# Kernel tuning notes

Measured on AMD Instinct MI355X. Metric: run time of the kernel, lower is better.

## Reference

```python
import jax, jax.numpy as jnp
import numpy as np

N = 100000   # nodes
E = 1600000  # edges (avg degree 16)
D = 64       # out_channels (in_channels == out_channels, so no zero-padding step)
L = 2        # GatedGraphConv num_layers


def setup_inputs() -> dict:
    key = jax.random.key(0)
    ks = jax.random.split(key, 11)
    w = lambda k, shape: jax.random.normal(k, shape, jnp.float32) * 0.05
    return {
        "x": jax.random.normal(ks[0], (N, D), jnp.float32),
        "edge_index": jax.random.randint(ks[1], (2, E), 0, N, dtype=jnp.int64),
        "conv_w": w(ks[2], (L, D, D)),        # GatedGraphConv per-layer message weight
        "gru_w_ih": w(ks[3], (3 * D, D)),     # GRUCell input->hidden (r|z|n)
        "gru_w_hh": w(ks[4], (3 * D, D)),     # GRUCell hidden->hidden (r|z|n)
        "gru_b_ih": w(ks[5], (3 * D,)),
        "gru_b_hh": w(ks[6], (3 * D,)),
        "lin_w": w(ks[7], (D, D)),            # nn.Linear(out, out)
        "lin_b": w(ks[8], (D,)),
        "attn_w": w(ks[9], (1, D)),           # nn.Linear(out, 1)
        "attn_b": w(ks[10], (1,)),
    }


def reference(x, edge_index, conv_w, gru_w_ih, gru_w_hh, gru_b_ih, gru_b_hh,
              lin_w, lin_b, attn_w, attn_b):
    src, dst = edge_index[0], edge_index[1]
    h = x  # in_channels == out_channels -> no padding
    for i in range(L):
        m = h @ conv_w[i]  # [N, D] transformed messages
        # gather at source nodes, scatter-add into target nodes
        agg = jax.ops.segment_sum(m[src], dst, num_segments=N)  # [N, D]
        # GRUCell(agg, h)
        gi = agg @ gru_w_ih.T + gru_b_ih  # [N, 3D]
        gh = h @ gru_w_hh.T + gru_b_hh    # [N, 3D]
        i_r, i_z, i_n = jnp.split(gi, 3, axis=1)
        h_r, h_z, h_n = jnp.split(gh, 3, axis=1)
        r = jax.nn.sigmoid(i_r + h_r)
        z = jax.nn.sigmoid(i_z + h_z)
        n = jnp.tanh(i_n + r * h_n)
        h = (1.0 - z) * n + z * h
    y = jax.nn.relu(h) @ lin_w.T + lin_b                 # [N, D]
    attn = jax.nn.softmax(y @ attn_w.T + attn_b, axis=0) # [N, 1], softmax over nodes
    return (attn * y).sum(axis=0, keepdims=True)          # [1, D]
```

## Files before the change

### kernel.cpp

```cpp
#include <hip/hip_runtime.h>


typedef __attribute__((ext_vector_type(8))) short s8v;
typedef __attribute__((ext_vector_type(4))) float f32x4;

#define CSR_CAP 12288
#define HSTR 136

__device__ __forceinline__ unsigned short f32_bf16_rn(float x) {
  unsigned u = __float_as_uint(x);
  u += 0x7FFF + ((u >> 16) & 1);
  return (unsigned short)(u >> 16);
}

__device__ __forceinline__ int wave_incl_scan(int v, int lane) {
#pragma unroll
  for (int d = 1; d < 64; d <<= 1) {
    int u = __shfl_up(v, d);
    if (lane >= d) v += u;
  }
  return v;
}

__device__ __forceinline__ int detect_is64(const int* ei, int E) {
  int nz = 0;
  int lim = (E < 512) ? E : 512;
  for (int i = threadIdx.x; i < lim; i += blockDim.x)
    nz |= (ei[2 * i + 1] != 0);
  return __syncthreads_or(nz) ? 0 : 1;
}

__device__ __forceinline__ void load_edge(const int* ei, int E, int is64,
                                          int e, int& s, int& d) {
  if (is64) { s = ei[2 * e]; d = ei[2 * (E + e)]; }
  else      { s = ei[e];     d = ei[E + e]; }
}

__global__ __launch_bounds__(256) void count_kernel(
    const int* __restrict__ ei, int E,
    int* __restrict__ G, int P, int perBlk, int NB) {
  __shared__ int hist[512];
  int tid = threadIdx.x, b = blockIdx.x;
  for (int i = tid; i < 512; i += 256) hist[i] = 0;
  int is64 = detect_is64(ei, E);
  __syncthreads();
  int e0 = b * perBlk, e1 = min(e0 + perBlk, E);
  for (int e = e0 + tid; e < e1; e += 256) {
    int s, d; load_edge(ei, E, is64, e, s, d);
    atomicAdd(&hist[d >> 8], 1);
  }
  __syncthreads();
  for (int i = tid; i < P; i += 256) G[i * NB + b] = hist[i];
}

__global__ __launch_bounds__(256) void scan2a(int* __restrict__ G,
                                              int* __restrict__ total, int NB) {
  __shared__ int wsum[4];
  int p = blockIdx.x, tid = threadIdx.x, lane = tid & 63, wv = tid >> 6;
  int v = G[p * NB + tid];
  int incl = wave_incl_scan(v, lane);
  if (lane == 63) wsum[wv] = incl;
  __syncthreads();
  if (tid == 0) {
    int a = wsum[0], b2 = wsum[1], c = wsum[2], d = wsum[3];
    total[p] = a + b2 + c + d;
    wsum[0] = 0; wsum[1] = a; wsum[2] = a + b2; wsum[3] = a + b2 + c;
  }
  __syncthreads();
  G[p * NB + tid] = incl - v + wsum[wv];
}

__global__ void scan2b(const int* __restrict__ total, int* __restrict__ partStart,
                       int P) {
  int lane = threadIdx.x;
  int running = 0;
  for (int base = 0; base < P; base += 64) {
    int idx = base + lane;
    int v = (idx < P) ? total[idx] : 0;
    int incl = wave_incl_scan(v, lane);
    int tot = __shfl(incl, 63);
    if (idx < P) partStart[idx] = running + incl - v;
    running += tot;
  }
  if (lane == 0) partStart[P] = running;
}

__global__ __launch_bounds__(256) void scatter_kernel(
    const int* __restrict__ ei, int E,
    const int* __restrict__ G, const int* __restrict__ partStart,
    int* __restrict__ bucket, int P, int perBlk, int NB) {
  __shared__ int cur[512];
  int tid = threadIdx.x, b = blockIdx.x;
  int is64 = detect_is64(ei, E);
  for (int i = tid; i < P; i += 256) cur[i] = partStart[i] + G[i * NB + b];
  __syncthreads();
  int e0 = b * perBlk, e1 = min(e0 + perBlk, E);
  for (int e = e0 + tid; e < e1; e += 256) {
    int s, d; load_edge(ei, E, is64, e, s, d);
    int pos = atomicAdd(&cur[d >> 8], 1);
    bucket[pos] = ((d & 255) << 17) | s;
  }
}

__global__ __launch_bounds__(256) void buildcsr_kernel(
    const int* __restrict__ partStart, const int* __restrict__ bucket,
    int* __restrict__ row_ptr, int* __restrict__ col, int N) {
  __shared__ int stage[CSR_CAP];
  __shared__ int hist[256];
  __shared__ int cur[256];
  __shared__ int wsum[4];
  int p = blockIdx.x, tid = threadIdx.x;
  int beg = partStart[p], end = partStart[p + 1];
  int cnt = end - beg;
  int base = p << 8;
  hist[tid] = 0;
  __syncthreads();
  bool staged = (cnt <= CSR_CAP);
  if (staged) {
    for (int i = tid; i < cnt; i += 256) {
      int v = bucket[beg + i];
      stage[i] = v;
      atomicAdd(&hist[(v >> 17) & 255], 1);
    }
  } else {
    for (int i = tid; i < cnt; i += 256)
      atomicAdd(&hist[(bucket[beg + i] >> 17) & 255], 1);
  }
  __syncthreads();
  int lane = tid & 63, wv = tid >> 6;
  int v = hist[tid];
  int incl = wave_incl_scan(v, lane);
  if (lane == 63) wsum[wv] = incl;
  __syncthreads();
  if (tid == 0) {
    int s0 = wsum[0], s1 = wsum[1], s2 = wsum[2];
    wsum[0] = 0; wsum[1] = s0; wsum[2] = s0 + s1; wsum[3] = s0 + s1 + s2;
  }
  __syncthreads();
  int excl = incl - v + wsum[wv];
  cur[tid] = beg + excl;
  if (base + tid < N) {
    if (tid == 0) row_ptr[base] = beg;
    row_ptr[base + tid + 1] = beg + excl + v;
  }
  __syncthreads();
  if (staged) {
    for (int i = tid; i < cnt; i += 256) {
      int v2 = stage[i];
      int pos = atomicAdd(&cur[(v2 >> 17) & 255], 1);
      col[pos] = v2 & 0x1FFFF;
    }
  } else {
    for (int i = tid; i < cnt; i += 256) {
      int v2 = bucket[beg + i];
      int pos = atomicAdd(&cur[(v2 >> 17) & 255], 1);
      col[pos] = v2 & 0x1FFFF;
    }
  }
}

__global__ void wprep_kernel(const float* __restrict__ conv_w,
                             const float* __restrict__ w_ih,
                             const float* __restrict__ whh,
                             const float* __restrict__ lin_w,
                             unsigned short* __restrict__ Bt,
                             unsigned short* __restrict__ Lt) {
  int idx = blockIdx.x * blockDim.x + threadIdx.x;
  if (idx < 65536) {
    int l = idx >> 15;
    int rr = idx & 32767;
    int cp = rr >> 7, p = rr & 127;
    int ch = cp >> 2, g = cp & 3;
    float val = 0.f;
    if (p < 64) {
      int j = (g == 0) ? ch : (g == 1) ? 64 + ch : (g == 2) ? 128 + ch : -1;
      if (j >= 0) {
        const float* C = conv_w + l * 4096 + p * 64;
        const float* W = w_ih + j * 64;
#pragma unroll 8
        for (int k = 0; k < 64; k++) val += C[k] * W[k];
      }
    } else {
      int q = p - 64;
      if (g == 0)      val = whh[ch * 64 + q];
      else if (g == 1) val = whh[(64 + ch) * 64 + q];
      else if (g == 3) val = whh[(128 + ch) * 64 + q];
    }
    Bt[(size_t)l * 32768 + (size_t)cp * 128 + p] = f32_bf16_rn(val);
  } else if (idx < 65536 + 4096) {
    int i2 = idx - 65536;
    float val = lin_w[i2];
    unsigned short hi = f32_bf16_rn(val);
    float fh = __uint_as_float((unsigned)hi << 16);
    unsigned short lo = f32_bf16_rn(val - fh);
    Lt[i2] = hi;
    Lt[4096 + i2] = lo;
  }
}

__global__ __launch_bounds__(256) void cvt16_kernel(
    const float* __restrict__ in, unsigned short* __restrict__ out, int n8) {
  int idx = blockIdx.x * blockDim.x + threadIdx.x;
  if (idx >= n8) return;
  const float4* p = (const float4*)(in + (size_t)idx * 8);
  float4 v0 = p[0], v1 = p[1];
  uint4 o;
  o.x = (unsigned)f32_bf16_rn(v0.x) | ((unsigned)f32_bf16_rn(v0.y) << 16);
  o.y = (unsigned)f32_bf16_rn(v0.z) | ((unsigned)f32_bf16_rn(v0.w) << 16);
  o.z = (unsigned)f32_bf16_rn(v1.x) | ((unsigned)f32_bf16_rn(v1.y) << 16);
  o.w = (unsigned)f32_bf16_rn(v1.z) | ((unsigned)f32_bf16_rn(v1.w) << 16);
  *(uint4*)(out + (size_t)idx * 8) = o;
}

__device__ __forceinline__ void acc_u2(unsigned rx, unsigned ry, float4& a) {
  a.x += __uint_as_float(rx << 16);
  a.y += __uint_as_float(rx & 0xFFFF0000u);
  a.z += __uint_as_float(ry << 16);
  a.w += __uint_as_float(ry & 0xFFFF0000u);
}

__global__ __launch_bounds__(256) void gather_kernel(
    const unsigned short* __restrict__ hb, const int* __restrict__ row_ptr,
    const int* __restrict__ col, unsigned short* __restrict__ sout,
    int N, int Em1) {
  int gt = blockIdx.x * blockDim.x + threadIdx.x;
  int n = gt >> 6, lane = gt & 63;
  if (n >= N) return;
  int grp = lane >> 4, q = lane & 15;
  int beg = row_ptr[n], end = row_ptr[n + 1];
  float4 acc = make_float4(0.f, 0.f, 0.f, 0.f);

  {
    int safe0 = min(beg, Em1);
    uint2 r[8];
    int idx[8];
#pragma unroll
    for (int i = 0; i < 8; i++) {
      int ee = beg + grp + 4 * i;
      idx[i] = (ee < end) ? ee : -1;
      int ci = (idx[i] >= 0) ? ee : safe0;
      int s = col[ci];
      r[i] = *(const uint2*)(hb + (size_t)s * 64 + q * 4);
    }
#pragma unroll
    for (int i = 0; i < 8; i++)
      if (idx[i] >= 0) acc_u2(r[i].x, r[i].y, acc);
  }
  for (int ee = beg + grp + 32; ee < end; ee += 4) {
    int s = col[ee];
    uint2 r = *(const uint2*)(hb + (size_t)s * 64 + q * 4);
    acc_u2(r.x, r.y, acc);
  }

#pragma unroll
  for (int off = 16; off <= 32; off <<= 1) {
    acc.x += __shfl_xor(acc.x, off);
    acc.y += __shfl_xor(acc.y, off);
    acc.z += __shfl_xor(acc.z, off);
    acc.w += __shfl_xor(acc.w, off);
  }
  if (grp == 0) {
    uint2 o;
    o.x = (unsigned)f32_bf16_rn(acc.x) | ((unsigned)f32_bf16_rn(acc.y) << 16);
    o.y = (unsigned)f32_bf16_rn(acc.z) | ((unsigned)f32_bf16_rn(acc.w) << 16);
    *(uint2*)(sout + (size_t)n * 64 + q * 4) = o;
  }
}

__global__ __launch_bounds__(512, 4) void gemm_gru_kernel(
    const unsigned short* __restrict__ s16,
    const unsigned short* __restrict__ h16in,
    unsigned short* __restrict__ h16out,
    const unsigned short* __restrict__ bt,
    const float* __restrict__ b_ih, const float* __restrict__ b_hh,
    int N, int ntiles) {
  __shared__ short Ahi[64 * HSTR];
  const int tid = threadIdx.x;
  const int lane = tid & 63, w = tid >> 6;
  const int l15 = lane & 15, ko = (lane >> 4) * 8;
  const int q = lane >> 4;

  s8v Bf[2][4];
#pragma unroll
  for (int ct = 0; ct < 2; ct++)
#pragma unroll
    for (int kk = 0; kk < 4; kk++)
      Bf[ct][kk] = *(const s8v*)(bt + (size_t)(32 * w + 16 * ct + l15) * 128 +
                                 kk * 32 + ko);

  const int ch0 = 8 * w + q, ch1 = ch0 + 4;
  const float br0 = b_ih[ch0] + b_hh[ch0], br1 = b_ih[ch1] + b_hh[ch1];
  const float bz0 = b_ih[64 + ch0] + b_hh[64 + ch0], bz1 = b_ih[64 + ch1] + b_hh[64 + ch1];
  const float bi0 = b_ih[128 + ch0], bi1 = b_ih[128 + ch1];
  const float bn0 = b_hh[128 + ch0], bn1 = b_hh[128 + ch1];

  const int g = tid >> 3, qc = tid & 7;

  for (int tile = blockIdx.x; tile < ntiles; tile += gridDim.x) {
    const int nb = tile * 64;
    const int node = nb + g;
    {
      uint4 sv = make_uint4(0, 0, 0, 0), hv = make_uint4(0, 0, 0, 0);
      if (node < N) {
        sv = *(const uint4*)(s16 + (size_t)node * 64 + qc * 8);
        hv = *(const uint4*)(h16in + (size_t)node * 64 + qc * 8);
      }
      *(uint4*)&Ahi[g * HSTR + qc * 8] = sv;
      *(uint4*)&Ahi[g * HSTR + 64 + qc * 8] = hv;
    }
    __syncthreads();

    f32x4 acc[4][2];
#pragma unroll
    for (int m = 0; m < 4; m++)
#pragma unroll
      for (int ct = 0; ct < 2; ct++) acc[m][ct] = (f32x4)(0.f);

#pragma unroll
    for (int m = 0; m < 4; m++) {
      const short* arh = &Ahi[(16 * m + l15) * HSTR + ko];
#pragma unroll
      for (int kk = 0; kk < 4; kk++) {
        s8v a_h = *(const s8v*)(arh + kk * 32);
#pragma unroll
        for (int ct = 0; ct < 2; ct++)
          acc[m][ct] = __builtin_amdgcn_mfma_f32_16x16x32_bf16(Bf[ct][kk], a_h, acc[m][ct], 0, 0, 0);
      }
    }

#pragma unroll
    for (int m = 0; m < 4; m++) {
      int loc = 16 * m + l15;
      int nd = nb + loc;
      if (nd < N) {
#pragma unroll
        for (int ct = 0; ct < 2; ct++) {
          int ch = ct ? ch1 : ch0;
          unsigned hu = (unsigned short)Ahi[loc * HSTR + 64 + ch];
          float hold = __uint_as_float(hu << 16);
          float rr = 1.f / (1.f + __expf(-(acc[m][ct][0] + (ct ? br1 : br0))));
          float zz = 1.f / (1.f + __expf(-(acc[m][ct][1] + (ct ? bz1 : bz0))));
          float narg = acc[m][ct][2] + (ct ? bi1 : bi0) +
                       rr * (acc[m][ct][3] + (ct ? bn1 : bn0));
          narg = fminf(fmaxf(narg, -15.f), 15.f);
          float t = __expf(2.f * narg);
          float nn = (t - 1.f) / (t + 1.f);
          float hv = (1.f - zz) * nn + zz * hold;
          h16out[(size_t)nd * 64 + ch] = f32_bf16_rn(hv);
        }
      }
    }
    __syncthreads();
  }
}

__device__ __forceinline__ unsigned relu_pk_bf16(unsigned v) {
  unsigned lo = (v & 0x00008000u) ? 0u : (v & 0x0000FFFFu);
  unsigned hi = (v & 0x80000000u) ? 0u : (v & 0xFFFF0000u);
  return lo | hi;
}

__global__ __launch_bounds__(256, 2) void final_mfma(
    const unsigned short* __restrict__ h16, const unsigned short* __restrict__ Lt,
    const float* __restrict__ lin_b, const float* __restrict__ attn_w,
    const float* __restrict__ attn_b, float* __restrict__ partials,
    int N, int ntiles) {
  __shared__ short Alds[64 * 72];
  __shared__ float red[4][64];
  __shared__ float pl[64];
  const int tid = threadIdx.x;
  const int lane = tid & 63, w = tid >> 6;
  const int l15 = lane & 15, ko = (lane >> 4) * 8;
  const int q = lane >> 4;

  s8v Lh[2], Ll[2];
  const int col = 16 * w + l15;
#pragma unroll
  for (int kk = 0; kk < 2; kk++) {
    Lh[kk] = *(const s8v*)(Lt + (size_t)col * 64 + kk * 32 + ko);
    Ll[kk] = *(const s8v*)(Lt + 4096 + (size_t)col * 64 + kk * 32 + ko);
  }
  const float lb = lin_b[col];
  const float aw = attn_w[col];
  const float ab = attn_b[0];
  const int sr = tid >> 2, part = tid & 3;

  float accS = 0.f;
  float accY = 0.f;

  for (int tile = blockIdx.x; tile < ntiles; tile += gridDim.x) {
    const int nb = tile * 64;
    {
      int node = nb + sr;
      uint4 v0 = make_uint4(0, 0, 0, 0), v1 = make_uint4(0, 0, 0, 0);
      if (node < N) {
        v0 = *(const uint4*)(h16 + (size_t)node * 64 + part * 16);
        v1 = *(const uint4*)(h16 + (size_t)node * 64 + part * 16 + 8);
      }
      v0.x = relu_pk_bf16(v0.x); v0.y = relu_pk_bf16(v0.y);
      v0.z = relu_pk_bf16(v0.z); v0.w = relu_pk_bf16(v0.w);
      v1.x = relu_pk_bf16(v1.x); v1.y = relu_pk_bf16(v1.y);
      v1.z = relu_pk_bf16(v1.z); v1.w = relu_pk_bf16(v1.w);
      short* ah = &Alds[sr * 72 + part * 16];
      *(uint4*)ah = v0;
      *(uint4*)(ah + 8) = v1;
    }
    __syncthreads();

    f32x4 acc[4];
#pragma unroll
    for (int m = 0; m < 4; m++) acc[m] = (f32x4)(0.f);
#pragma unroll
    for (int m = 0; m < 4; m++) {
      const short* arow = &Alds[(16 * m + l15) * 72 + ko];
#pragma unroll
      for (int kk = 0; kk < 2; kk++) {
        s8v a_h = *(const s8v*)(arow + kk * 32);
        acc[m] = __builtin_amdgcn_mfma_f32_16x16x32_bf16(a_h, Lh[kk], acc[m], 0, 0, 0);
        acc[m] = __builtin_amdgcn_mfma_f32_16x16x32_bf16(a_h, Ll[kk], acc[m], 0, 0, 0);
      }
    }
    __syncthreads();

    float cc[4][4];
#pragma unroll
    for (int m = 0; m < 4; m++)
#pragma unroll
      for (int g = 0; g < 4; g++) cc[m][g] = (acc[m][g] + lb) * aw;
#pragma unroll
    for (int off = 1; off <= 8; off <<= 1)
#pragma unroll
      for (int m = 0; m < 4; m++)
#pragma unroll
        for (int g = 0; g < 4; g++) cc[m][g] += __shfl_xor(cc[m][g], off);
    if (l15 == 0) {
#pragma unroll
      for (int m = 0; m < 4; m++)
#pragma unroll
        for (int g = 0; g < 4; g++) red[w][16 * m + 4 * q + g] = cc[m][g];
    }
    __syncthreads();
    if (tid < 64) {
      float t = red[0][tid] + red[1][tid] + red[2][tid] + red[3][tid] + ab;
      float p = (nb + tid < N) ? __expf(t) : 0.f;
      pl[tid] = p;
      accS += p;
    }
    __syncthreads();
#pragma unroll
    for (int m = 0; m < 4; m++)
#pragma unroll
      for (int g = 0; g < 4; g++)
        accY += pl[16 * m + 4 * q + g] * (acc[m][g] + lb);
  }

  accY += __shfl_xor(accY, 16);
  accY += __shfl_xor(accY, 32);
  if (lane < 16) partials[(size_t)blockIdx.x * 66 + 16 * w + lane] = accY;
  if (w == 0) {
    float s = accS;
#pragma unroll
    for (int off = 1; off < 64; off <<= 1) s += __shfl_xor(s, off);
    if (lane == 0) partials[(size_t)blockIdx.x * 66 + 64] = s;
  }
}

__global__ void final_p2(const float* __restrict__ partials,
                         float* __restrict__ out, int nb) {
  __shared__ float red[16][65];
  int tid = threadIdx.x;
  int j = tid & 63, grp = tid >> 6;
  float sy = 0.f, ss = 0.f;
  for (int b = grp; b < nb; b += 16) {
    sy += partials[b * 66 + j];
    if (j == 0) ss += partials[b * 66 + 64];
  }
  red[grp][j] = sy;
  if (j == 0) red[grp][64] = ss;
  __syncthreads();
  if (tid < 64) {
    float Y = 0.f, S = 0.f;
#pragma unroll
    for (int i = 0; i < 16; i++) { Y += red[i][tid]; S += red[i][64]; }
    out[tid] = Y / S;
  }
}

extern "C" void kernel_launch(void* const* d_in, const int* in_sizes, int n_in,
                              void* d_out, int out_size, void* d_ws, size_t ws_size,
                              hipStream_t stream) {
  const float* x       = (const float*)d_in[0];
  const int*   ei      = (const int*)d_in[1];
  const float* conv_w  = (const float*)d_in[2];
  const float* gw_ih   = (const float*)d_in[3];
  const float* gw_hh   = (const float*)d_in[4];
  const float* gb_ih   = (const float*)d_in[5];
  const float* gb_hh   = (const float*)d_in[6];
  const float* lin_w   = (const float*)d_in[7];
  const float* lin_b   = (const float*)d_in[8];
  const float* attn_w  = (const float*)d_in[9];
  const float* attn_b  = (const float*)d_in[10];
  float* out = (float*)d_out;

  const int N = in_sizes[0] / 64;
  const int E = in_sizes[1] / 2;
  const int P  = (N + 255) >> 8;
  const int NB = 256;
  const int perBlk = (E + NB - 1) / NB;

  char* ws = (char*)d_ws;
  size_t off = 0;
  auto alloc = [&](size_t bytes) {
    void* p = ws + off;
    off = (off + bytes + 255) & ~(size_t)255;
    return p;
  };
  int*   G         = (int*)alloc((size_t)P * NB * 4);
  int*   total     = (int*)alloc((size_t)P * 4);
  int*   partStart = (int*)alloc((size_t)(P + 1) * 4);
  int*   bucket    = (int*)alloc((size_t)E * 4);
  int*   row_ptr   = (int*)alloc((size_t)(N + 1) * 4);
  int*   colb      = (int*)alloc((size_t)E * 4);
  unsigned short* Bt  = (unsigned short*)alloc(2 * 256 * 128 * 2);
  unsigned short* Lt  = (unsigned short*)alloc(2 * 4096 * 2);
  unsigned short* b16x = (unsigned short*)alloc((size_t)N * 64 * 2);
  unsigned short* b16h = (unsigned short*)alloc((size_t)N * 64 * 2);
  unsigned short* s16  = (unsigned short*)alloc((size_t)N * 64 * 2);
  float* partials  = (float*)alloc(1024 * 66 * 4);
  if (off > ws_size) return;

  count_kernel<<<NB, 256, 0, stream>>>(ei, E, G, P, perBlk, NB);
  scan2a<<<P, 256, 0, stream>>>(G, total, NB);
  scan2b<<<1, 64, 0, stream>>>(total, partStart, P);
  scatter_kernel<<<NB, 256, 0, stream>>>(ei, E, G, partStart, bucket, P, perBlk, NB);
  buildcsr_kernel<<<P, 256, 0, stream>>>(partStart, bucket, row_ptr, colb, N);
  wprep_kernel<<<(65536 + 4096 + 255) / 256, 256, 0, stream>>>(conv_w, gw_ih, gw_hh,
                                                               lin_w, Bt, Lt);
  int n8 = (N * 64) / 8;
  cvt16_kernel<<<(n8 + 255) / 256, 256, 0, stream>>>(x, b16x, n8);

  int gb = (N * 64 + 255) / 256;
  int ntiles = (N + 63) / 64;
  gather_kernel<<<gb, 256, 0, stream>>>(b16x, row_ptr, colb, s16, N, E - 1);
  gemm_gru_kernel<<<1024, 512, 0, stream>>>(s16, b16x, b16h, Bt,
                                            gb_ih, gb_hh, N, ntiles);
  gather_kernel<<<gb, 256, 0, stream>>>(b16h, row_ptr, colb, s16, N, E - 1);
  gemm_gru_kernel<<<1024, 512, 0, stream>>>(s16, b16h, b16h, Bt + 32768,
                                            gb_ih, gb_hh, N, ntiles);
  final_mfma<<<512, 256, 0, stream>>>(b16h, Lt, lin_b, attn_w, attn_b, partials, N, ntiles);
  final_p2<<<1, 1024, 0, stream>>>(partials, out, 512);
}
```

Baseline: 217.3 us.

## Double-buffer GRU GEMM tile loads via global_load_lds and fuse tail kernels

New measurement: 250.8 us. +15.4%, slower.

```diff
diff --git a/kernel.cpp b/kernel.cpp
--- a/kernel.cpp
+++ b/kernel.cpp
@@ -5,7 +5,6 @@
 typedef __attribute__((ext_vector_type(4))) float f32x4;
 
 #define CSR_CAP 12288
-#define HSTR 136
 
 __device__ __forceinline__ unsigned short f32_bf16_rn(float x) {
   unsigned u = __float_as_uint(x);
@@ -38,9 +37,10 @@
 
 __global__ __launch_bounds__(256) void count_kernel(
     const int* __restrict__ ei, int E,
-    int* __restrict__ G, int P, int perBlk, int NB) {
+    int* __restrict__ G, int P, int perBlk, int NB, int* __restrict__ dcnt) {
   __shared__ int hist[512];
   int tid = threadIdx.x, b = blockIdx.x;
+  if (b == 0 && tid < 2) dcnt[tid] = 0;
   for (int i = tid; i < 512; i += 256) hist[i] = 0;
   int is64 = detect_is64(ei, E);
   __syncthreads();
@@ -54,8 +54,12 @@
 }
 
 __global__ __launch_bounds__(256) void scan2a(int* __restrict__ G,
-                                              int* __restrict__ total, int NB) {
+                                              int* __restrict__ total,
+                                              int* __restrict__ partStart,
+                                              int NB, int P,
+                                              int* __restrict__ dcnt) {
   __shared__ int wsum[4];
+  __shared__ int amLast;
   int p = blockIdx.x, tid = threadIdx.x, lane = tid & 63, wv = tid >> 6;
   int v = G[p * NB + tid];
   int incl = wave_incl_scan(v, lane);
@@ -68,21 +72,23 @@
   }
   __syncthreads();
   G[p * NB + tid] = incl - v + wsum[wv];
-}
-
-__global__ void scan2b(const int* __restrict__ total, int* __restrict__ partStart,
-                       int P) {
-  int lane = threadIdx.x;
-  int running = 0;
-  for (int base = 0; base < P; base += 64) {
-    int idx = base + lane;
-    int v = (idx < P) ? total[idx] : 0;
-    int incl = wave_incl_scan(v, lane);
-    int tot = __shfl(incl, 63);
-    if (idx < P) partStart[idx] = running + incl - v;
-    running += tot;
-  }
-  if (lane == 0) partStart[P] = running;
+  if (tid == 0) {
+    __threadfence();
+    amLast = (atomicAdd(&dcnt[0], 1) == P - 1);
+  }
+  __syncthreads();
+  if (amLast && tid < 64) {
+    int running = 0;
+    for (int base = 0; base < P; base += 64) {
+      int idx = base + lane;
+      int vv = (idx < P) ? total[idx] : 0;
+      int ii = wave_incl_scan(vv, lane);
+      int tot = __shfl(ii, 63);
+      if (idx < P) partStart[idx] = running + ii - vv;
+      running += tot;
+    }
+    if (lane == 0) partStart[P] = running;
+  }
 }
 
 __global__ __launch_bounds__(256) void scatter_kernel(
@@ -163,8 +169,10 @@
                              const float* __restrict__ w_ih,
                              const float* __restrict__ whh,
                              const float* __restrict__ lin_w,
+                             const float* __restrict__ x,
                              unsigned short* __restrict__ Bt,
-                             unsigned short* __restrict__ Lt) {
+                             unsigned short* __restrict__ Lt,
+                             unsigned short* __restrict__ x16, int n8) {
   int idx = blockIdx.x * blockDim.x + threadIdx.x;
   if (idx < 65536) {
     int l = idx >> 15;
@@ -195,21 +203,19 @@
     unsigned short lo = f32_bf16_rn(val - fh);
     Lt[i2] = hi;
     Lt[4096 + i2] = lo;
-  }
-}
-
-__global__ __launch_bounds__(256) void cvt16_kernel(
-    const float* __restrict__ in, unsigned short* __restrict__ out, int n8) {
-  int idx = blockIdx.x * blockDim.x + threadIdx.x;
-  if (idx >= n8) return;
-  const float4* p = (const float4*)(in + (size_t)idx * 8);
-  float4 v0 = p[0], v1 = p[1];
-  uint4 o;
-  o.x = (unsigned)f32_bf16_rn(v0.x) | ((unsigned)f32_bf16_rn(v0.y) << 16);
-  o.y = (unsigned)f32_bf16_rn(v0.z) | ((unsigned)f32_bf16_rn(v0.w) << 16);
-  o.z = (unsigned)f32_bf16_rn(v1.x) | ((unsigned)f32_bf16_rn(v1.y) << 16);
-  o.w = (unsigned)f32_bf16_rn(v1.z) | ((unsigned)f32_bf16_rn(v1.w) << 16);
-  *(uint4*)(out + (size_t)idx * 8) = o;
+  } else {
+    int i2 = idx - (65536 + 4096);
+    if (i2 < n8) {
+      const float4* pp = (const float4*)(x + (size_t)i2 * 8);
+      float4 v0 = pp[0], v1 = pp[1];
+      uint4 o;
+      o.x = (unsigned)f32_bf16_rn(v0.x) | ((unsigned)f32_bf16_rn(v0.y) << 16);
+      o.y = (unsigned)f32_bf16_rn(v0.z) | ((unsigned)f32_bf16_rn(v0.w) << 16);
+      o.z = (unsigned)f32_bf16_rn(v1.x) | ((unsigned)f32_bf16_rn(v1.y) << 16);
+      o.w = (unsigned)f32_bf16_rn(v1.z) | ((unsigned)f32_bf16_rn(v1.w) << 16);
+      *(uint4*)(x16 + (size_t)i2 * 8) = o;
+    }
+  }
 }
 
 __device__ __forceinline__ void acc_u2(unsigned rx, unsigned ry, float4& a) {
@@ -274,7 +280,7 @@
     const unsigned short* __restrict__ bt,
     const float* __restrict__ b_ih, const float* __restrict__ b_hh,
     int N, int ntiles) {
-  __shared__ short Ahi[64 * HSTR];
+  __shared__ short Alds[2 * 8192];
   const int tid = threadIdx.x;
   const int lane = tid & 63, w = tid >> 6;
   const int l15 = lane & 15, ko = (lane >> 4) * 8;
@@ -294,21 +300,36 @@
   const float bi0 = b_ih[128 + ch0], bi1 = b_ih[128 + ch1];
   const float bn0 = b_hh[128 + ch0], bn1 = b_hh[128 + ch1];
 
-  const int g = tid >> 3, qc = tid & 7;
-
-  for (int tile = blockIdx.x; tile < ntiles; tile += gridDim.x) {
-    const int nb = tile * 64;
-    const int node = nb + g;
-    {
-      uint4 sv = make_uint4(0, 0, 0, 0), hv = make_uint4(0, 0, 0, 0);
-      if (node < N) {
-        sv = *(const uint4*)(s16 + (size_t)node * 64 + qc * 8);
-        hv = *(const uint4*)(h16in + (size_t)node * 64 + qc * 8);
-      }
-      *(uint4*)&Ahi[g * HSTR + qc * 8] = sv;
-      *(uint4*)&Ahi[g * HSTR + 64 + qc * 8] = hv;
-    }
+  const int lrow = lane >> 3;
+  const int schk = (lane & 7) ^ lrow;
+  const int stride = gridDim.x;
+
+  auto issue_loads = [&](int tile, int buf) {
+    int node = min(tile * 64 + 8 * w + lrow, N - 1);
+    const unsigned short* gs = s16 + (size_t)node * 64 + schk * 8;
+    const unsigned short* gh = h16in + (size_t)node * 64 + schk * 8;
+    short* ds = &Alds[buf * 8192 + w * 512];
+    short* dh = &Alds[buf * 8192 + 4096 + w * 512];
+    __builtin_amdgcn_global_load_lds(
+        (const __attribute__((address_space(1))) void*)gs,
+        (__attribute__((address_space(3))) void*)ds, 16, 0, 0);
+    __builtin_amdgcn_global_load_lds(
+        (const __attribute__((address_space(1))) void*)gh,
+        (__attribute__((address_space(3))) void*)dh, 16, 0, 0);
+  };
+
+  const int tile0 = blockIdx.x;
+  if (tile0 < ntiles) issue_loads(tile0, 0);
+  int cur = 0;
+
+  for (int tile = tile0; tile < ntiles; tile += stride) {
     __syncthreads();
+    const int nxt = tile + stride;
+    if (nxt < ntiles) issue_loads(nxt, cur ^ 1);
+
+    const short* sp = &Alds[cur * 8192];
+    const short* hp = sp + 4096;
+    const int rx = l15 & 7;
 
     f32x4 acc[4][2];
 #pragma unroll
@@ -318,16 +339,19 @@
 
 #pragma unroll
     for (int m = 0; m < 4; m++) {
-      const short* arh = &Ahi[(16 * m + l15) * HSTR + ko];
+      const int r = 16 * m + l15;
 #pragma unroll
       for (int kk = 0; kk < 4; kk++) {
-        s8v a_h = *(const s8v*)(arh + kk * 32);
+        const short* base = (kk < 2) ? sp : hp;
+        int cc = (((kk & 1) * 4 + q) ^ rx);
+        s8v a_h = *(const s8v*)(base + r * 64 + cc * 8);
 #pragma unroll
         for (int ct = 0; ct < 2; ct++)
           acc[m][ct] = __builtin_amdgcn_mfma_f32_16x16x32_bf16(Bf[ct][kk], a_h, acc[m][ct], 0, 0, 0);
       }
     }
 
+    const int nb = tile * 64;
 #pragma unroll
     for (int m = 0; m < 4; m++) {
       int loc = 16 * m + l15;
@@ -336,7 +360,8 @@
 #pragma unroll
         for (int ct = 0; ct < 2; ct++) {
           int ch = ct ? ch1 : ch0;
-          unsigned hu = (unsigned short)Ahi[loc * HSTR + 64 + ch];
+          int hcc = (ch >> 3) ^ rx;
+          unsigned hu = (unsigned short)hp[loc * 64 + hcc * 8 + (ch & 7)];
           float hold = __uint_as_float(hu << 16);
           float rr = 1.f / (1.f + __expf(-(acc[m][ct][0] + (ct ? br1 : br0))));
           float zz = 1.f / (1.f + __expf(-(acc[m][ct][1] + (ct ? bz1 : bz0))));
@@ -350,7 +375,7 @@
         }
       }
     }
-    __syncthreads();
+    cur ^= 1;
   }
 }
 
@@ -364,10 +389,11 @@
     const unsigned short* __restrict__ h16, const unsigned short* __restrict__ Lt,
     const float* __restrict__ lin_b, const float* __restrict__ attn_w,
     const float* __restrict__ attn_b, float* __restrict__ partials,
-    int N, int ntiles) {
+    float* __restrict__ out, int* __restrict__ dcnt, int N, int ntiles) {
   __shared__ short Alds[64 * 72];
   __shared__ float red[4][64];
   __shared__ float pl[64];
+  __shared__ int amLast;
   const int tid = threadIdx.x;
   const int lane = tid & 63, w = tid >> 6;
   const int l15 = lane & 15, ko = (lane >> 4) * 8;
@@ -463,26 +489,28 @@
     for (int off = 1; off < 64; off <<= 1) s += __shfl_xor(s, off);
     if (lane == 0) partials[(size_t)blockIdx.x * 66 + 64] = s;
   }
-}
-
-__global__ void final_p2(const float* __restrict__ partials,
-                         float* __restrict__ out, int nb) {
-  __shared__ float red[16][65];
-  int tid = threadIdx.x;
-  int j = tid & 63, grp = tid >> 6;
-  float sy = 0.f, ss = 0.f;
-  for (int b = grp; b < nb; b += 16) {
-    sy += partials[b * 66 + j];
-    if (j == 0) ss += partials[b * 66 + 64];
-  }
-  red[grp][j] = sy;
-  if (j == 0) red[grp][64] = ss;
-  __syncthreads();
-  if (tid < 64) {
-    float Y = 0.f, S = 0.f;
-#pragma unroll
-    for (int i = 0; i < 16; i++) { Y += red[i][tid]; S += red[i][64]; }
-    out[tid] = Y / S;
+
+  if (tid == 0) {
+    __threadfence();
+    amLast = (atomicAdd(&dcnt[1], 1) == (int)gridDim.x - 1);
+  }
+  __syncthreads();
+  if (amLast) {
+    __shared__ float red2[4][65];
+    int grp = tid >> 6, j = tid & 63;
+    float sy = 0.f, ss = 0.f;
+    for (int b = grp; b < (int)gridDim.x; b += 4) {
+      sy += partials[(size_t)b * 66 + j];
+      if (j == 0) ss += partials[(size_t)b * 66 + 64];
+    }
+    red2[grp][j] = sy;
+    if (j == 0) red2[grp][64] = ss;
+    __syncthreads();
+    if (tid < 64) {
+      float Y = red2[0][tid] + red2[1][tid] + red2[2][tid] + red2[3][tid];
+      float S = red2[0][64] + red2[1][64] + red2[2][64] + red2[3][64];
+      out[tid] = Y / S;
+    }
   }
 }
 
@@ -521,6 +549,7 @@
   int*   bucket    = (int*)alloc((size_t)E * 4);
   int*   row_ptr   = (int*)alloc((size_t)(N + 1) * 4);
   int*   colb      = (int*)alloc((size_t)E * 4);
+  int*   dcnt      = (int*)alloc(256);
   unsigned short* Bt  = (unsigned short*)alloc(2 * 256 * 128 * 2);
   unsigned short* Lt  = (unsigned short*)alloc(2 * 4096 * 2);
   unsigned short* b16x = (unsigned short*)alloc((size_t)N * 64 * 2);
@@ -529,15 +558,13 @@
   float* partials  = (float*)alloc(1024 * 66 * 4);
   if (off > ws_size) return;
 
-  count_kernel<<<NB, 256, 0, stream>>>(ei, E, G, P, perBlk, NB);
-  scan2a<<<P, 256, 0, stream>>>(G, total, NB);
-  scan2b<<<1, 64, 0, stream>>>(total, partStart, P);
+  count_kernel<<<NB, 256, 0, stream>>>(ei, E, G, P, perBlk, NB, dcnt);
+  scan2a<<<P, 256, 0, stream>>>(G, total, partStart, NB, P, dcnt);
   scatter_kernel<<<NB, 256, 0, stream>>>(ei, E, G, partStart, bucket, P, perBlk, NB);
   buildcsr_kernel<<<P, 256, 0, stream>>>(partStart, bucket, row_ptr, colb, N);
-  wprep_kernel<<<(65536 + 4096 + 255) / 256, 256, 0, stream>>>(conv_w, gw_ih, gw_hh,
-                                                               lin_w, Bt, Lt);
   int n8 = (N * 64) / 8;
-  cvt16_kernel<<<(n8 + 255) / 256, 256, 0, stream>>>(x, b16x, n8);
+  wprep_kernel<<<(65536 + 4096 + n8 + 255) / 256, 256, 0, stream>>>(
+      conv_w, gw_ih, gw_hh, lin_w, x, Bt, Lt, b16x, n8);
 
   int gb = (N * 64 + 255) / 256;
   int ntiles = (N + 63) / 64;
@@ -547,6 +574,6 @@
   gather_kernel<<<gb, 256, 0, stream>>>(b16h, row_ptr, colb, s16, N, E - 1);
   gemm_gru_kernel<<<1024, 512, 0, stream>>>(s16, b16h, b16h, Bt + 32768,
                                             gb_ih, gb_hh, N, ntiles);
-  final_mfma<<<512, 256, 0, stream>>>(b16h, Lt, lin_b, attn_w, attn_b, partials, N, ntiles);
-  final_p2<<<1, 1024, 0, stream>>>(partials, out, 512);
-}
+  final_mfma<<<512, 256, 0, stream>>>(b16h, Lt, lin_b, attn_w, attn_b,
+                                      partials, out, dcnt, N, ntiles);
+}
```

## Fold final linear layer through attention sum and fuse small prep kernels

Applied to the files above, without the earlier changes.

New measurement: 229.3 us. 5.5% more time.

```diff
diff --git a/kernel.cpp b/kernel.cpp
--- a/kernel.cpp
+++ b/kernel.cpp
@@ -38,9 +38,10 @@
 
 __global__ __launch_bounds__(256) void count_kernel(
     const int* __restrict__ ei, int E,
-    int* __restrict__ G, int P, int perBlk, int NB) {
+    int* __restrict__ G, int P, int perBlk, int NB, int* __restrict__ dcnt) {
   __shared__ int hist[512];
   int tid = threadIdx.x, b = blockIdx.x;
+  if (b == 0 && tid == 0) dcnt[0] = 0;
   for (int i = tid; i < 512; i += 256) hist[i] = 0;
   int is64 = detect_is64(ei, E);
   __syncthreads();
@@ -54,8 +55,12 @@
 }
 
 __global__ __launch_bounds__(256) void scan2a(int* __restrict__ G,
-                                              int* __restrict__ total, int NB) {
+                                              int* __restrict__ total,
+                                              int* __restrict__ partStart,
+                                              int NB, int P,
+                                              int* __restrict__ dcnt) {
   __shared__ int wsum[4];
+  __shared__ int amLast;
   int p = blockIdx.x, tid = threadIdx.x, lane = tid & 63, wv = tid >> 6;
   int v = G[p * NB + tid];
   int incl = wave_incl_scan(v, lane);
@@ -68,21 +73,23 @@
   }
   __syncthreads();
   G[p * NB + tid] = incl - v + wsum[wv];
-}
-
-__global__ void scan2b(const int* __restrict__ total, int* __restrict__ partStart,
-                       int P) {
-  int lane = threadIdx.x;
-  int running = 0;
-  for (int base = 0; base < P; base += 64) {
-    int idx = base + lane;
-    int v = (idx < P) ? total[idx] : 0;
-    int incl = wave_incl_scan(v, lane);
-    int tot = __shfl(incl, 63);
-    if (idx < P) partStart[idx] = running + incl - v;
-    running += tot;
-  }
-  if (lane == 0) partStart[P] = running;
+  if (tid == 0) {
+    __threadfence();
+    amLast = (atomicAdd(&dcnt[0], 1) == P - 1);
+  }
+  __syncthreads();
+  if (amLast && tid < 64) {
+    int running = 0;
+    for (int base = 0; base < P; base += 64) {
+      int idx = base + lane;
+      int vv = (idx < P) ? total[idx] : 0;
+      int ii = wave_incl_scan(vv, lane);
+      int tot = __shfl(ii, 63);
+      if (idx < P) partStart[idx] = running + ii - vv;
+      running += tot;
+    }
+    if (lane == 0) partStart[P] = running;
+  }
 }
 
 __global__ __launch_bounds__(256) void scatter_kernel(
@@ -163,8 +170,11 @@
                              const float* __restrict__ w_ih,
                              const float* __restrict__ whh,
                              const float* __restrict__ lin_w,
+                             const float* __restrict__ attn_w,
+                             const float* __restrict__ x,
                              unsigned short* __restrict__ Bt,
-                             unsigned short* __restrict__ Lt) {
+                             float* __restrict__ uf,
+                             unsigned short* __restrict__ x16, int n8) {
   int idx = blockIdx.x * blockDim.x + threadIdx.x;
   if (idx < 65536) {
     int l = idx >> 15;
@@ -187,29 +197,25 @@
       else if (g == 3) val = whh[(128 + ch) * 64 + q];
     }
     Bt[(size_t)l * 32768 + (size_t)cp * 128 + p] = f32_bf16_rn(val);
-  } else if (idx < 65536 + 4096) {
-    int i2 = idx - 65536;
-    float val = lin_w[i2];
-    unsigned short hi = f32_bf16_rn(val);
-    float fh = __uint_as_float((unsigned)hi << 16);
-    unsigned short lo = f32_bf16_rn(val - fh);
-    Lt[i2] = hi;
-    Lt[4096 + i2] = lo;
-  }
-}
-
-__global__ __launch_bounds__(256) void cvt16_kernel(
-    const float* __restrict__ in, unsigned short* __restrict__ out, int n8) {
-  int idx = blockIdx.x * blockDim.x + threadIdx.x;
-  if (idx >= n8) return;
-  const float4* p = (const float4*)(in + (size_t)idx * 8);
-  float4 v0 = p[0], v1 = p[1];
-  uint4 o;
-  o.x = (unsigned)f32_bf16_rn(v0.x) | ((unsigned)f32_bf16_rn(v0.y) << 16);
-  o.y = (unsigned)f32_bf16_rn(v0.z) | ((unsigned)f32_bf16_rn(v0.w) << 16);
-  o.z = (unsigned)f32_bf16_rn(v1.x) | ((unsigned)f32_bf16_rn(v1.y) << 16);
-  o.w = (unsigned)f32_bf16_rn(v1.z) | ((unsigned)f32_bf16_rn(v1.w) << 16);
-  *(uint4*)(out + (size_t)idx * 8) = o;
+  } else if (idx < 65536 + 64) {
+    int k = idx - 65536;
+    float acc = 0.f;
+#pragma unroll 8
+    for (int c = 0; c < 64; c++) acc += attn_w[c] * lin_w[c * 64 + k];
+    uf[k] = acc;
+  } else if (idx >= 65792) {
+    int i2 = idx - 65792;
+    if (i2 < n8) {
+      const float4* pp = (const float4*)(x + (size_t)i2 * 8);
+      float4 v0 = pp[0], v1 = pp[1];
+      uint4 o;
+      o.x = (unsigned)f32_bf16_rn(v0.x) | ((unsigned)f32_bf16_rn(v0.y) << 16);
+      o.y = (unsigned)f32_bf16_rn(v0.z) | ((unsigned)f32_bf16_rn(v0.w) << 16);
+      o.z = (unsigned)f32_bf16_rn(v1.x) | ((unsigned)f32_bf16_rn(v1.y) << 16);
+      o.w = (unsigned)f32_bf16_rn(v1.z) | ((unsigned)f32_bf16_rn(v1.w) << 16);
+      *(uint4*)(x16 + (size_t)i2 * 8) = o;
+    }
+  }
 }
 
 __device__ __forceinline__ void acc_u2(unsigned rx, unsigned ry, float4& a) {
@@ -360,129 +366,96 @@
   return lo | hi;
 }
 
-__global__ __launch_bounds__(256, 2) void final_mfma(
-    const unsigned short* __restrict__ h16, const unsigned short* __restrict__ Lt,
-    const float* __restrict__ lin_b, const float* __restrict__ attn_w,
-    const float* __restrict__ attn_b, float* __restrict__ partials,
-    int N, int ntiles) {
-  __shared__ short Alds[64 * 72];
-  __shared__ float red[4][64];
-  __shared__ float pl[64];
-  const int tid = threadIdx.x;
-  const int lane = tid & 63, w = tid >> 6;
-  const int l15 = lane & 15, ko = (lane >> 4) * 8;
-  const int q = lane >> 4;
-
-  s8v Lh[2], Ll[2];
-  const int col = 16 * w + l15;
-#pragma unroll
-  for (int kk = 0; kk < 2; kk++) {
-    Lh[kk] = *(const s8v*)(Lt + (size_t)col * 64 + kk * 32 + ko);
-    Ll[kk] = *(const s8v*)(Lt + 4096 + (size_t)col * 64 + kk * 32 + ko);
-  }
-  const float lb = lin_b[col];
-  const float aw = attn_w[col];
-  const float ab = attn_b[0];
-  const int sr = tid >> 2, part = tid & 3;
-
+__global__ __launch_bounds__(256) void attn_stream(
+    const unsigned short* __restrict__ h16, const float* __restrict__ u,
+    float* __restrict__ partials, int N) {
+  __shared__ float zb[4][64];
+  __shared__ float sb[4];
+  int tid = threadIdx.x, lane = tid & 63, wv = tid >> 6;
+  int g = lane >> 3, c8 = lane & 7;
+  float u8[8];
+#pragma unroll
+  for (int i = 0; i < 8; i++) u8[i] = u[c8 * 8 + i];
+  float accY[8];
+#pragma unroll
+  for (int i = 0; i < 8; i++) accY[i] = 0.f;
   float accS = 0.f;
-  float accY = 0.f;
-
-  for (int tile = blockIdx.x; tile < ntiles; tile += gridDim.x) {
-    const int nb = tile * 64;
-    {
-      int node = nb + sr;
-      uint4 v0 = make_uint4(0, 0, 0, 0), v1 = make_uint4(0, 0, 0, 0);
-      if (node < N) {
-        v0 = *(const uint4*)(h16 + (size_t)node * 64 + part * 16);
-        v1 = *(const uint4*)(h16 + (size_t)node * 64 + part * 16 + 8);
-      }
-      v0.x = relu_pk_bf16(v0.x); v0.y = relu_pk_bf16(v0.y);
-      v0.z = relu_pk_bf16(v0.z); v0.w = relu_pk_bf16(v0.w);
-      v1.x = relu_pk_bf16(v1.x); v1.y = relu_pk_bf16(v1.y);
-      v1.z = relu_pk_bf16(v1.z); v1.w = relu_pk_bf16(v1.w);
-      short* ah = &Alds[sr * 72 + part * 16];
-      *(uint4*)ah = v0;
-      *(uint4*)(ah + 8) = v1;
-    }
-    __syncthreads();
-
-    f32x4 acc[4];
-#pragma unroll
-    for (int m = 0; m < 4; m++) acc[m] = (f32x4)(0.f);
-#pragma unroll
-    for (int m = 0; m < 4; m++) {
-      const short* arow = &Alds[(16 * m + l15) * 72 + ko];
-#pragma unroll
-      for (int kk = 0; kk < 2; kk++) {
-        s8v a_h = *(const s8v*)(arow + kk * 32);
-        acc[m] = __builtin_amdgcn_mfma_f32_16x16x32_bf16(a_h, Lh[kk], acc[m], 0, 0, 0);
-        acc[m] = __builtin_amdgcn_mfma_f32_16x16x32_bf16(a_h, Ll[kk], acc[m], 0, 0, 0);
-      }
-    }
-    __syncthreads();
-
-    float cc[4][4];
-#pragma unroll
-    for (int m = 0; m < 4; m++)
-#pragma unroll
-      for (int g = 0; g < 4; g++) cc[m][g] = (acc[m][g] + lb) * aw;
-#pragma unroll
-    for (int off = 1; off <= 8; off <<= 1)
-#pragma unroll
-      for (int m = 0; m < 4; m++)
-#pragma unroll
-        for (int g = 0; g < 4; g++) cc[m][g] += __shfl_xor(cc[m][g], off);
-    if (l15 == 0) {
-#pragma unroll
-      for (int m = 0; m < 4; m++)
-#pragma unroll
-        for (int g = 0; g < 4; g++) red[w][16 * m + 4 * q + g] = cc[m][g];
-    }
-    __syncthreads();
-    if (tid < 64) {
-      float t = red[0][tid] + red[1][tid] + red[2][tid] + red[3][tid] + ab;
-      float p = (nb + tid < N) ? __expf(t) : 0.f;
-      pl[tid] = p;
-      accS += p;
-    }
-    __syncthreads();
-#pragma unroll
-    for (int m = 0; m < 4; m++)
-#pragma unroll
-      for (int g = 0; g < 4; g++)
-        accY += pl[16 * m + 4 * q + g] * (acc[m][g] + lb);
-  }
-
-  accY += __shfl_xor(accY, 16);
-  accY += __shfl_xor(accY, 32);
-  if (lane < 16) partials[(size_t)blockIdx.x * 66 + 16 * w + lane] = accY;
-  if (w == 0) {
-    float s = accS;
-#pragma unroll
-    for (int off = 1; off < 64; off <<= 1) s += __shfl_xor(s, off);
-    if (lane == 0) partials[(size_t)blockIdx.x * 66 + 64] = s;
+  int wave = blockIdx.x * 4 + wv;
+  int nwaves = gridDim.x * 4;
+  for (int nb = wave * 8; nb < N; nb += nwaves * 8) {
+    int node = nb + g;
+    uint4 hv = make_uint4(0, 0, 0, 0);
+    if (node < N) hv = *(const uint4*)(h16 + (size_t)node * 64 + c8 * 8);
+    unsigned words[4] = {hv.x, hv.y, hv.z, hv.w};
+    float f[8];
+#pragma unroll
+    for (int i2 = 0; i2 < 4; i2++) {
+      unsigned v = relu_pk_bf16(words[i2]);
+      f[2 * i2]     = __uint_as_float(v << 16);
+      f[2 * i2 + 1] = __uint_as_float(v & 0xFFFF0000u);
+    }
+    float t = 0.f;
+#pragma unroll
+    for (int i = 0; i < 8; i++) t += f[i] * u8[i];
+    t += __shfl_xor(t, 1);
+    t += __shfl_xor(t, 2);
+    t += __shfl_xor(t, 4);
+    float p = (node < N) ? __expf(t) : 0.f;
+    if (c8 == 0) accS += p;
+#pragma unroll
+    for (int i = 0; i < 8; i++) accY[i] += p * f[i];
+  }
+#pragma unroll
+  for (int off = 8; off <= 32; off <<= 1) {
+#pragma unroll
+    for (int i = 0; i < 8; i++) accY[i] += __shfl_xor(accY[i], off);
+    accS += __shfl_xor(accS, off);
+  }
+  if (lane < 8) {
+#pragma unroll
+    for (int i = 0; i < 8; i++) zb[wv][lane * 8 + i] = accY[i];
+    if (lane == 0) sb[wv] = accS;
+  }
+  __syncthreads();
+  if (tid < 64) {
+    float z = zb[0][tid] + zb[1][tid] + zb[2][tid] + zb[3][tid];
+    partials[(size_t)blockIdx.x * 65 + tid] = z;
+    if (tid == 0)
+      partials[(size_t)blockIdx.x * 65 + 64] = sb[0] + sb[1] + sb[2] + sb[3];
   }
 }
 
 __global__ void final_p2(const float* __restrict__ partials,
+                         const float* __restrict__ lin_w,
+                         const float* __restrict__ lin_b,
                          float* __restrict__ out, int nb) {
   __shared__ float red[16][65];
+  __shared__ float zf[64];
+  __shared__ float Sf;
   int tid = threadIdx.x;
   int j = tid & 63, grp = tid >> 6;
   float sy = 0.f, ss = 0.f;
   for (int b = grp; b < nb; b += 16) {
-    sy += partials[b * 66 + j];
-    if (j == 0) ss += partials[b * 66 + 64];
+    sy += partials[(size_t)b * 65 + j];
+    if (j == 0) ss += partials[(size_t)b * 65 + 64];
   }
   red[grp][j] = sy;
   if (j == 0) red[grp][64] = ss;
   __syncthreads();
   if (tid < 64) {
-    float Y = 0.f, S = 0.f;
-#pragma unroll
-    for (int i = 0; i < 16; i++) { Y += red[i][tid]; S += red[i][64]; }
-    out[tid] = Y / S;
+    float z = 0.f, S = 0.f;
+#pragma unroll
+    for (int i = 0; i < 16; i++) { z += red[i][tid]; S += red[i][64]; }
+    zf[tid] = z;
+    if (tid == 0) Sf = S;
+  }
+  __syncthreads();
+  if (tid < 64) {
+    float acc = 0.f;
+    const float* wrow = lin_w + tid * 64;
+#pragma unroll 8
+    for (int k = 0; k < 64; k++) acc += zf[k] * wrow[k];
+    out[tid] = acc / Sf + lin_b[tid];
   }
 }
 
@@ -521,23 +494,22 @@
   int*   bucket    = (int*)alloc((size_t)E * 4);
   int*   row_ptr   = (int*)alloc((size_t)(N + 1) * 4);
   int*   colb      = (int*)alloc((size_t)E * 4);
+  int*   dcnt      = (int*)alloc(256);
   unsigned short* Bt  = (unsigned short*)alloc(2 * 256 * 128 * 2);
-  unsigned short* Lt  = (unsigned short*)alloc(2 * 4096 * 2);
+  float* uf        = (float*)alloc(64 * 4);
   unsigned short* b16x = (unsigned short*)alloc((size_t)N * 64 * 2);
   unsigned short* b16h = (unsigned short*)alloc((size_t)N * 64 * 2);
   unsigned short* s16  = (unsigned short*)alloc((size_t)N * 64 * 2);
-  float* partials  = (float*)alloc(1024 * 66 * 4);
+  float* partials  = (float*)alloc(1024 * 65 * 4);
   if (off > ws_size) return;
 
-  count_kernel<<<NB, 256, 0, stream>>>(ei, E, G, P, perBlk, NB);
-  scan2a<<<P, 256, 0, stream>>>(G, total, NB);
-  scan2b<<<1, 64, 0, stream>>>(total, partStart, P);
+  count_kernel<<<NB, 256, 0, stream>>>(ei, E, G, P, perBlk, NB, dcnt);
+  scan2a<<<P, 256, 0, stream>>>(G, total, partStart, NB, P, dcnt);
   scatter_kernel<<<NB, 256, 0, stream>>>(ei, E, G, partStart, bucket, P, perBlk, NB);
   buildcsr_kernel<<<P, 256, 0, stream>>>(partStart, bucket, row_ptr, colb, N);
-  wprep_kernel<<<(65536 + 4096 + 255) / 256, 256, 0, stream>>>(conv_w, gw_ih, gw_hh,
-                                                               lin_w, Bt, Lt);
   int n8 = (N * 64) / 8;
-  cvt16_kernel<<<(n8 + 255) / 256, 256, 0, stream>>>(x, b16x, n8);
+  wprep_kernel<<<(65792 + n8 + 255) / 256, 256, 0, stream>>>(
+      conv_w, gw_ih, gw_hh, lin_w, attn_w, x, Bt, uf, b16x, n8);
 
   int gb = (N * 64 + 255) / 256;
   int ntiles = (N + 63) / 64;
@@ -547,6 +519,6 @@
   gather_kernel<<<gb, 256, 0, stream>>>(b16h, row_ptr, colb, s16, N, E - 1);
   gemm_gru_kernel<<<1024, 512, 0, stream>>>(s16, b16h, b16h, Bt + 32768,
                                             gb_ih, gb_hh, N, ntiles);
-  final_mfma<<<512, 256, 0, stream>>>(b16h, Lt, lin_b, attn_w, attn_b, partials, N, ntiles);
-  final_p2<<<1, 1024, 0, stream>>>(partials, out, 512);
-}
+  attn_stream<<<1024, 256, 0, stream>>>(b16h, uf, partials, N);
+  final_p2<<<1, 1024, 0, stream>>>(partials, lin_w, lin_b, out, 1024);
+}
```
